# Performance work log

Measured on AMD Instinct MI355X. Metric: run time of the kernel, lower is better.

Reference implementation:

```python
import jax, jax.numpy as jnp
import numpy as np


def _bce_logits(x, t):
    # numerically stable BCEWithLogits (pos_weight=1), elementwise
    return jnp.maximum(x, 0.0) - x * t + jnp.log1p(jnp.exp(-jnp.abs(x)))


def _ciou(box1, box2, eps=1e-9):
    # box1, box2: [n,4] in (cx, cy, w, h); matches bbox_iou(..., x1y1x2y2=False, CIoU=True)
    b1x1, b1x2 = box1[:, 0] - box1[:, 2] / 2, box1[:, 0] + box1[:, 2] / 2
    b1y1, b1y2 = box1[:, 1] - box1[:, 3] / 2, box1[:, 1] + box1[:, 3] / 2
    b2x1, b2x2 = box2[:, 0] - box2[:, 2] / 2, box2[:, 0] + box2[:, 2] / 2
    b2y1, b2y2 = box2[:, 1] - box2[:, 3] / 2, box2[:, 1] + box2[:, 3] / 2
    inter = (jnp.clip(jnp.minimum(b1x2, b2x2) - jnp.maximum(b1x1, b2x1), 0.0)
             * jnp.clip(jnp.minimum(b1y2, b2y2) - jnp.maximum(b1y1, b2y1), 0.0))
    w1, h1 = b1x2 - b1x1, b1y2 - b1y1 + eps
    w2, h2 = b2x2 - b2x1, b2y2 - b2y1 + eps
    union = w1 * h1 + w2 * h2 - inter + eps
    iou = inter / union
    cw = jnp.maximum(b1x2, b2x2) - jnp.minimum(b1x1, b2x1)
    ch = jnp.maximum(b1y2, b2y2) - jnp.minimum(b1y1, b2y1)
    c2 = cw ** 2 + ch ** 2 + eps
    rho2 = ((b2x1 + b2x2 - b1x1 - b1x2) ** 2 + (b2y1 + b2y2 - b1y1 - b1y2) ** 2) / 4.0
    v = (4.0 / jnp.pi ** 2) * (jnp.arctan(w2 / h2) - jnp.arctan(w1 / h1)) ** 2
    alpha = jax.lax.stop_gradient(v / (1.0 + eps - iou + v))  # torch.no_grad()
    return iou - (rho2 / c2 + v * alpha)


def _layer_loss(preds, targets, anchors, li):
    # preds: [B, na, H, W, 5+nc]; targets: [nt,6]; anchors: [n_layers, na, 2]
    B, na, H, W, C = preds.shape
    nt = targets.shape[0]
    ai = jnp.arange(na, dtype=preds.dtype)
    # targets.repeat(na,1,1) with anchor index appended -> [na, nt, 7]
    t7 = jnp.concatenate([jnp.broadcast_to(targets[None], (na, nt, 6)),
                          jnp.broadcast_to(ai[:, None, None], (na, nt, 1))], axis=2)
    gain = jnp.array([1.0, 1.0, W, H, W, H, 1.0], dtype=preds.dtype)
    t = t7 * gain
    # anchor-ratio filter: max(r, 1/r).max(-1) < 4 (as boolean mask instead of fancy-index)
    r = t[:, :, 4:6] / anchors[li][:, None, :]                  # [na, nt, 2]
    mask = jnp.max(jnp.maximum(r, 1.0 / r), axis=2) < 4.0       # [na, nt]
    tf = t.reshape(na * nt, 7)
    m = mask.reshape(-1)
    mf = m.astype(preds.dtype)
    b = tf[:, 0].astype(jnp.int32)
    c = tf[:, 1].astype(jnp.int32)
    gxy = tf[:, 2:4]
    gwh = tf[:, 4:6]
    gij = gxy.astype(jnp.int32)  # .long() truncation (coords >= 0)
    gi = jnp.clip(gij[:, 0], 0, W - 1)
    gj = jnp.clip(gij[:, 1], 0, H - 1)
    a = tf[:, 6].astype(jnp.int32)
    # faithful to original: anch = anchors[a] then forward takes [range(n), a] => anchors[a, a]
    anch = anchors[a, a]
    # img_ids = unique(batch ids).flip(); with full 0..B-1 coverage lookup == B-1-b
    match = (B - 1) - b
    ps = preds[match, a, gj, gi]                                # [na*nt, C] gather
    pxy = jax.nn.sigmoid(ps[:, :2])
    pwh = jnp.exp(ps[:, 2:4]) * anch
    pbox = jnp.concatenate([pxy, pwh], axis=1)
    tbox = jnp.concatenate([gxy - gij.astype(gxy.dtype), gwh], axis=1)
    iou = _ciou(pbox, tbox)
    nvalid = jnp.maximum(mf.sum(), 1.0)
    lbox = ((1.0 - iou) * mf).sum() / nvalid                    # mean over matched targets
    # scatter detached clamped iou into tobj; invalid rows get OOB batch idx -> dropped
    scatter_b = jnp.where(m, match, B)
    tobj = jnp.zeros((B, na, H, W), preds.dtype).at[scatter_b, a, gj, gi].set(
        jax.lax.stop_gradient(jnp.clip(iou, 0.0)) * mf)
    nc = C - 5
    t1h = jax.nn.one_hot(c, nc, dtype=preds.dtype)
    lcls = (_bce_logits(ps[:, 5:], t1h) * mf[:, None]).sum() / (nvalid * nc)
    lobj = _bce_logits(preds[..., 4], tobj).mean()
    return lbox, lobj, lcls


def setup_inputs() -> dict:
    key = jax.random.key(0)
    ks = jax.random.split(key, 6)
    p0 = jax.random.normal(ks[0], (16, 3, 80, 80, 85), jnp.float32)
    p1 = jax.random.normal(ks[1], (16, 3, 40, 40, 85), jnp.float32)
    p2 = jax.random.normal(ks[2], (16, 3, 20, 20, 85), jnp.float32)
    nt, B = 300, 16
    img = (jnp.arange(nt) % B).astype(jnp.float32)  # every batch id present
    cls = jax.random.randint(ks[3], (nt,), 0, 80).astype(jnp.float32)
    xy = jax.random.uniform(ks[4], (nt, 2), minval=0.05, maxval=0.95)
    wh = jax.random.uniform(ks[5], (nt, 2), minval=0.02, maxval=0.2)
    targets = jnp.concatenate([img[:, None], cls[:, None], xy, wh], axis=1)
    anchors = jnp.array([[[1.25, 1.625], [2.0, 3.75], [4.125, 2.875]],
                         [[1.875, 3.8125], [3.875, 2.8125], [3.6875, 7.4375]],
                         [[3.625, 2.8125], [4.875, 6.1875], [11.65625, 10.1875]]],
                        dtype=jnp.float32)
    return {"p0": p0, "p1": p1, "p2": p2, "targets": targets, "anchors": anchors}


def reference(p0, p1, p2, targets, anchors):
    lb = lo = lc = 0.0
    for li, p in enumerate((p0, p1, p2)):
        a_, b_, c_ = _layer_loss(p, targets, anchors, li)
        lb = lb + a_
        lo = lo + b_
        lc = lc + c_
    lbox = lb * 0.05
    lobj = lo * 1.0
    lcls = lc * 0.5
    loss = lbox + lobj + lcls
    stats = jnp.stack([lbox, lobj, lcls, loss])
    return (jnp.reshape(loss, (1,)), stats)
```

## Files before the change

kernel.cpp:

```cpp
#include <hip/hip_runtime.h>
#include <math.h>

#define NT    300
#define NA    3
#define BATCH 16
#define NCLS  80
#define CCH   85
#define NROWS 2700
#define NBO   394
#define NBT   675
#define NBLK  (NBO + NBT)
#define HASHSZ 4096


__device__ __forceinline__ float softplusf(float x) {
    return fmaxf(x, 0.f) + log1pf(expf(-fabsf(x)));
}

__device__ __forceinline__ double block_reduce(double v, double* red) {
    #pragma unroll
    for (int off = 32; off > 0; off >>= 1) v += __shfl_down(v, off, 64);
    const int wid = threadIdx.x >> 6, lane = threadIdx.x & 63;
    if (lane == 0) red[wid] = v;
    __syncthreads();
    double r = (threadIdx.x < 4) ? red[threadIdx.x] : 0.0;
    r += __shfl_down(r, 2, 64);
    r += __shfl_down(r, 1, 64);
    __syncthreads();
    return r;
}

__global__ __launch_bounds__(256) void main_kernel(
    const float* __restrict__ p0, const float* __restrict__ p1,
    const float* __restrict__ p2,
    const float* __restrict__ targets, const float* __restrict__ anchors,
    char* __restrict__ ws)
{
    __shared__ double red[4];

    double* obj_part = (double*)(ws);
    float*  row_lbox = (float*)(ws + 3200);
    float*  row_lcls = (float*)(ws + 14000);
    float*  row_nval = (float*)(ws + 24800);
    int*    row_key  = (int*)(ws + 35600);
    float*  row_val  = (float*)(ws + 46400);

    if (blockIdx.x < NBO) {
        const int ob = blockIdx.x;
        int li, bb;
        if (ob < 300)      { li = 0; bb = ob; }
        else if (ob < 375) { li = 1; bb = ob - 300; }
        else               { li = 2; bb = ob - 375; }
        const float* p = (li == 0) ? p0 : ((li == 1) ? p1 : p2);
        const int N = (BATCH * NA * 6400) >> (2*li);

        float s = 0.f;
        #pragma unroll
        for (int k = 0; k < 4; ++k) {
            const int idx = bb * 1024 + k * 256 + threadIdx.x;
            if (idx < N) s += softplusf(p[(size_t)idx * CCH + 4]);
        }
        const double t = block_reduce((double)s, red);
        if (threadIdx.x == 0) obj_part[ob] = t;
        return;
    }

    const int gr   = (blockIdx.x - NBO) * 4 + (threadIdx.x >> 6);
    const int lane = threadIdx.x & 63;
    const int li   = gr / (NA * NT);
    const int r    = gr - li * (NA * NT);
    const int a    = r / NT;
    const int ti   = r - a * NT;
    const float* p = (li == 0) ? p0 : ((li == 1) ? p1 : p2);
    const int W = 80 >> li, H = W;

    const float img = targets[ti*6 + 0];
    const float cls = targets[ti*6 + 1];
    const float tx  = targets[ti*6 + 2] * (float)W;
    const float ty  = targets[ti*6 + 3] * (float)H;
    const float tw  = targets[ti*6 + 4] * (float)W;
    const float th  = targets[ti*6 + 5] * (float)H;

    const float ax = anchors[(li*3 + a)*2 + 0];
    const float ay = anchors[(li*3 + a)*2 + 1];
    const float rx = tw / ax, ry = th / ay;
    const float mr = fmaxf(fmaxf(rx, 1.f/rx), fmaxf(ry, 1.f/ry));
    const bool  mask = mr < 4.f;
    const float mf = mask ? 1.f : 0.f;

    const int b = (int)img;
    const int c = (int)cls;
    const int gij_x = (int)tx;
    const int gij_y = (int)ty;
    const int gi = min(max(gij_x, 0), W - 1);
    const int gj = min(max(gij_y, 0), H - 1);

    const float anch_x = anchors[(a*3 + a)*2 + 0];
    const float anch_y = anchors[(a*3 + a)*2 + 1];

    const int match = BATCH - 1 - b;
    const int cell  = ((match*NA + a)*H + gj)*W + gi;
    const float* ps = p + (size_t)cell * CCH;

    const float x1 = ps[lane];
    const float x2 = (lane < CCH - 64) ? ps[64 + lane] : 0.f;

    const float s0   = __shfl(x1, 0);
    const float s1   = __shfl(x1, 1);
    const float s2   = __shfl(x1, 2);
    const float s3   = __shfl(x1, 3);
    const float objx = __shfl(x1, 4);

    const int ch = 5 + c;
    float contrib = (lane >= 5) ? softplusf(x1) : 0.f;
    if (lane < CCH - 64) contrib += softplusf(x2);
    if (lane == ch) contrib -= x1;
    if (ch >= 64 && lane == ch - 64) contrib -= x2;
    #pragma unroll
    for (int off = 32; off > 0; off >>= 1)
        contrib += __shfl_down(contrib, off, 64);

    const float pxx = 1.f / (1.f + expf(-s0));
    const float pyy = 1.f / (1.f + expf(-s1));
    const float pw  = expf(s2) * anch_x;
    const float ph  = expf(s3) * anch_y;
    const float fx  = tx - (float)gij_x;
    const float fy  = ty - (float)gij_y;

    const float eps = 1e-9f;
    const float b1x1 = pxx - pw*0.5f, b1x2 = pxx + pw*0.5f;
    const float b1y1 = pyy - ph*0.5f, b1y2 = pyy + ph*0.5f;
    const float b2x1 = fx - tw*0.5f,  b2x2 = fx + tw*0.5f;
    const float b2y1 = fy - th*0.5f,  b2y2 = fy + th*0.5f;
    float iw = fminf(b1x2, b2x2) - fmaxf(b1x1, b2x1); iw = fmaxf(iw, 0.f);
    float ih = fminf(b1y2, b2y2) - fmaxf(b1y1, b2y1); ih = fmaxf(ih, 0.f);
    const float inter = iw * ih;
    const float w1 = b1x2 - b1x1, h1 = b1y2 - b1y1 + eps;
    const float w2 = b2x2 - b2x1, h2 = b2y2 - b2y1 + eps;
    const float uni = w1*h1 + w2*h2 - inter + eps;
    const float iou = inter / uni;
    const float cw  = fmaxf(b1x2, b2x2) - fminf(b1x1, b2x1);
    const float chh = fmaxf(b1y2, b2y2) - fminf(b1y1, b2y1);
    const float c2 = cw*cw + chh*chh + eps;
    const float dx = b2x1 + b2x2 - b1x1 - b1x2;
    const float dy = b2y1 + b2y2 - b1y1 - b1y2;
    const float rho2 = (dx*dx + dy*dy) * 0.25f;
    const float dat = atanf(w2/h2) - atanf(w1/h1);
    const float v = 0.40528473456935108577f * dat * dat;
    const float alpha = v / (1.f + eps - iou + v);
    const float ciou = iou - (rho2/c2 + v*alpha);

    if (lane == 0) {
        row_lbox[gr] = (1.f - ciou) * mf;
        row_lcls[gr] = contrib * mf;
        row_nval[gr] = mf;
        row_key[gr]  = mask ? ((li << 20) | cell) : -1;
        row_val[gr]  = mask ? objx * fmaxf(ciou, 0.f) : 0.f;
    }
}

__global__ __launch_bounds__(256) void final_kernel(
    const char* __restrict__ ws, float* __restrict__ out)
{
    __shared__ double red[4];
    __shared__ int hkey[HASHSZ];
    __shared__ int hrow[HASHSZ];

    const double* obj_part = (const double*)(ws);
    const float*  row_lbox = (const float*)(ws + 3200);
    const float*  row_lcls = (const float*)(ws + 14000);
    const float*  row_nval = (const float*)(ws + 24800);
    const int*    row_key  = (const int*)(ws + 35600);
    const float*  row_val  = (const float*)(ws + 46400);

    for (int q = threadIdx.x; q < HASHSZ; q += 256) { hkey[q] = -1; hrow[q] = -1; }
    __syncthreads();

    double so[3] = {0, 0, 0};
    for (int bk = threadIdx.x; bk < NBO; bk += 256) {
        const double v = obj_part[bk];
        if (bk < 300)      so[0] += v;
        else if (bk < 375) so[1] += v;
        else               so[2] += v;
    }

    int    slots[11];
    int    nm = 0;
    double lb[3] = {0,0,0}, lc[3] = {0,0,0}, nv[3] = {0,0,0}, co[3] = {0,0,0};

    for (int i = threadIdx.x; i < NROWS; i += 256) {
        const int l = i / (NA * NT);
        lb[l] += (double)row_lbox[i];
        lc[l] += (double)row_lcls[i];
        nv[l] += (double)row_nval[i];
        const int k = row_key[i];
        int s = -1;
        if (k >= 0) {
            unsigned h = ((unsigned)k * 2654435761u) >> 20;
            s = (int)(h & (HASHSZ - 1));
            while (true) {
                const int prev = atomicCAS(&hkey[s], -1, k);
                if (prev == -1 || prev == k) { atomicMax(&hrow[s], i); break; }
                s = (s + 1) & (HASHSZ - 1);
            }
        }
        slots[nm++] = s;
    }
    __syncthreads();
    nm = 0;
    for (int i = threadIdx.x; i < NROWS; i += 256) {
        const int s = slots[nm++];
        if (s >= 0 && hrow[s] == i)
            co[i / (NA * NT)] += (double)row_val[i];
    }

    double rsum[12];
    #pragma unroll
    for (int l = 0; l < 3; ++l) {
        rsum[l*4 + 0] = block_reduce(lb[l], red);
        rsum[l*4 + 1] = block_reduce(lc[l], red);
        rsum[l*4 + 2] = block_reduce(co[l], red);
        rsum[l*4 + 3] = block_reduce(nv[l], red);
        so[l]         = block_reduce(so[l], red);
    }

    if (threadIdx.x == 0) {
        double lbox = 0.0, lobj = 0.0, lcls = 0.0;
        for (int l = 0; l < 3; ++l) {
            const double nvv = fmax(rsum[l*4 + 3], 1.0);
            lbox += rsum[l*4 + 0] / nvv;
            lcls += rsum[l*4 + 1] / (nvv * (double)NCLS);
            const double N = (double)((BATCH * NA * 6400) >> (2*l));
            lobj += (so[l] - rsum[l*4 + 2]) / N;
        }
        lbox *= 0.05;
        lcls *= 0.5;
        const double loss = lbox + lobj + lcls;
        out[0] = (float)loss;
        out[1] = (float)lbox;
        out[2] = (float)lobj;
        out[3] = (float)lcls;
        out[4] = (float)loss;
    }
}

extern "C" void kernel_launch(void* const* d_in, const int* in_sizes, int n_in,
                              void* d_out, int out_size, void* d_ws, size_t ws_size,
                              hipStream_t stream) {
    const float* p0      = (const float*)d_in[0];
    const float* p1      = (const float*)d_in[1];
    const float* p2      = (const float*)d_in[2];
    const float* targets = (const float*)d_in[3];
    const float* anchors = (const float*)d_in[4];

    main_kernel<<<NBLK, 256, 0, stream>>>(p0, p1, p2, targets, anchors,
                                          (char*)d_ws);
    final_kernel<<<1, 256, 0, stream>>>((const char*)d_ws, (float*)d_out);
}
```

Before: 182.1 us.

## Merge row work into objectness blocks, pack row data, widen final kernel

Removes the separate row blocks: each of the 394 objectness blocks now also runs up to two target rows per wave after its objectness reduction. Per-row outputs are packed into one float4 plus a key, which cuts the number of global stores and loads. The final single-block kernel grows from 256 to 1024 threads so each thread handles fewer rows and hash insertions. The cost is a longer critical path per block in the main kernel, and 1024-thread reductions with more synchronisation in the final kernel.

```diff
diff --git a/kernel.cpp b/kernel.cpp
--- a/kernel.cpp
+++ b/kernel.cpp
@@ -7,9 +7,8 @@
 #define NCLS  80
 #define CCH   85
 #define NROWS 2700
-#define NBO   394
-#define NBT   675
-#define NBLK  (NBO + NBT)
+#define NBLK  394
+#define NWAVE (NBLK * 4)
 #define HASHSZ 4096
 
 
@@ -17,7 +16,7 @@
     return fmaxf(x, 0.f) + log1pf(expf(-fabsf(x)));
 }
 
-__device__ __forceinline__ double block_reduce(double v, double* red) {
+__device__ __forceinline__ double block_reduce256(double v, double* red) {
     #pragma unroll
     for (int off = 32; off > 0; off >>= 1) v += __shfl_down(v, off, 64);
     const int wid = threadIdx.x >> 6, lane = threadIdx.x & 63;
@@ -26,6 +25,19 @@
     double r = (threadIdx.x < 4) ? red[threadIdx.x] : 0.0;
     r += __shfl_down(r, 2, 64);
     r += __shfl_down(r, 1, 64);
+    __syncthreads();
+    return r;
+}
+
+__device__ __forceinline__ double block_reduce1024(double v, double* red) {
+    #pragma unroll
+    for (int off = 32; off > 0; off >>= 1) v += __shfl_down(v, off, 64);
+    const int wid = threadIdx.x >> 6, lane = threadIdx.x & 63;
+    if (lane == 0) red[wid] = v;
+    __syncthreads();
+    double r = (threadIdx.x < 16) ? red[threadIdx.x] : 0.0;
+    #pragma unroll
+    for (int off = 8; off > 0; off >>= 1) r += __shfl_down(r, off, 64);
     __syncthreads();
     return r;
 }
@@ -39,13 +51,10 @@
     __shared__ double red[4];
 
     double* obj_part = (double*)(ws);
-    float*  row_lbox = (float*)(ws + 3200);
-    float*  row_lcls = (float*)(ws + 14000);
-    float*  row_nval = (float*)(ws + 24800);
-    int*    row_key  = (int*)(ws + 35600);
-    float*  row_val  = (float*)(ws + 46400);
-
-    if (blockIdx.x < NBO) {
+    float4* row_data = (float4*)(ws + 3200);
+    int*    row_key  = (int*)(ws + 46400);
+
+    {
         const int ob = blockIdx.x;
         int li, bb;
         if (ob < 300)      { li = 0; bb = ob; }
@@ -60,139 +69,144 @@
             const int idx = bb * 1024 + k * 256 + threadIdx.x;
             if (idx < N) s += softplusf(p[(size_t)idx * CCH + 4]);
         }
-        const double t = block_reduce((double)s, red);
+        const double t = block_reduce256((double)s, red);
         if (threadIdx.x == 0) obj_part[ob] = t;
-        return;
-    }
-
-    const int gr   = (blockIdx.x - NBO) * 4 + (threadIdx.x >> 6);
+    }
+
+    const int gw   = blockIdx.x * 4 + (threadIdx.x >> 6);
     const int lane = threadIdx.x & 63;
-    const int li   = gr / (NA * NT);
-    const int r    = gr - li * (NA * NT);
-    const int a    = r / NT;
-    const int ti   = r - a * NT;
-    const float* p = (li == 0) ? p0 : ((li == 1) ? p1 : p2);
-    const int W = 80 >> li, H = W;
-
-    const float img = targets[ti*6 + 0];
-    const float cls = targets[ti*6 + 1];
-    const float tx  = targets[ti*6 + 2] * (float)W;
-    const float ty  = targets[ti*6 + 3] * (float)H;
-    const float tw  = targets[ti*6 + 4] * (float)W;
-    const float th  = targets[ti*6 + 5] * (float)H;
-
-    const float ax = anchors[(li*3 + a)*2 + 0];
-    const float ay = anchors[(li*3 + a)*2 + 1];
-    const float rx = tw / ax, ry = th / ay;
-    const float mr = fmaxf(fmaxf(rx, 1.f/rx), fmaxf(ry, 1.f/ry));
-    const bool  mask = mr < 4.f;
-    const float mf = mask ? 1.f : 0.f;
-
-    const int b = (int)img;
-    const int c = (int)cls;
-    const int gij_x = (int)tx;
-    const int gij_y = (int)ty;
-    const int gi = min(max(gij_x, 0), W - 1);
-    const int gj = min(max(gij_y, 0), H - 1);
-
-    const float anch_x = anchors[(a*3 + a)*2 + 0];
-    const float anch_y = anchors[(a*3 + a)*2 + 1];
-
-    const int match = BATCH - 1 - b;
-    const int cell  = ((match*NA + a)*H + gj)*W + gi;
-    const float* ps = p + (size_t)cell * CCH;
-
-    const float x1 = ps[lane];
-    const float x2 = (lane < CCH - 64) ? ps[64 + lane] : 0.f;
-
-    const float s0   = __shfl(x1, 0);
-    const float s1   = __shfl(x1, 1);
-    const float s2   = __shfl(x1, 2);
-    const float s3   = __shfl(x1, 3);
-    const float objx = __shfl(x1, 4);
-
-    const int ch = 5 + c;
-    float contrib = (lane >= 5) ? softplusf(x1) : 0.f;
-    if (lane < CCH - 64) contrib += softplusf(x2);
-    if (lane == ch) contrib -= x1;
-    if (ch >= 64 && lane == ch - 64) contrib -= x2;
-    #pragma unroll
-    for (int off = 32; off > 0; off >>= 1)
-        contrib += __shfl_down(contrib, off, 64);
-
-    const float pxx = 1.f / (1.f + expf(-s0));
-    const float pyy = 1.f / (1.f + expf(-s1));
-    const float pw  = expf(s2) * anch_x;
-    const float ph  = expf(s3) * anch_y;
-    const float fx  = tx - (float)gij_x;
-    const float fy  = ty - (float)gij_y;
-
-    const float eps = 1e-9f;
-    const float b1x1 = pxx - pw*0.5f, b1x2 = pxx + pw*0.5f;
-    const float b1y1 = pyy - ph*0.5f, b1y2 = pyy + ph*0.5f;
-    const float b2x1 = fx - tw*0.5f,  b2x2 = fx + tw*0.5f;
-    const float b2y1 = fy - th*0.5f,  b2y2 = fy + th*0.5f;
-    float iw = fminf(b1x2, b2x2) - fmaxf(b1x1, b2x1); iw = fmaxf(iw, 0.f);
-    float ih = fminf(b1y2, b2y2) - fmaxf(b1y1, b2y1); ih = fmaxf(ih, 0.f);
-    const float inter = iw * ih;
-    const float w1 = b1x2 - b1x1, h1 = b1y2 - b1y1 + eps;
-    const float w2 = b2x2 - b2x1, h2 = b2y2 - b2y1 + eps;
-    const float uni = w1*h1 + w2*h2 - inter + eps;
-    const float iou = inter / uni;
-    const float cw  = fmaxf(b1x2, b2x2) - fminf(b1x1, b2x1);
-    const float chh = fmaxf(b1y2, b2y2) - fminf(b1y1, b2y1);
-    const float c2 = cw*cw + chh*chh + eps;
-    const float dx = b2x1 + b2x2 - b1x1 - b1x2;
-    const float dy = b2y1 + b2y2 - b1y1 - b1y2;
-    const float rho2 = (dx*dx + dy*dy) * 0.25f;
-    const float dat = atanf(w2/h2) - atanf(w1/h1);
-    const float v = 0.40528473456935108577f * dat * dat;
-    const float alpha = v / (1.f + eps - iou + v);
-    const float ciou = iou - (rho2/c2 + v*alpha);
-
-    if (lane == 0) {
-        row_lbox[gr] = (1.f - ciou) * mf;
-        row_lcls[gr] = contrib * mf;
-        row_nval[gr] = mf;
-        row_key[gr]  = mask ? ((li << 20) | cell) : -1;
-        row_val[gr]  = mask ? objx * fmaxf(ciou, 0.f) : 0.f;
-    }
-}
-
-__global__ __launch_bounds__(256) void final_kernel(
+
+    #pragma unroll
+    for (int rr = 0; rr < 2; ++rr) {
+        const int gr = gw + rr * NWAVE;
+        if (gr >= NROWS) break;
+        const int li = gr / (NA * NT);
+        const int r  = gr - li * (NA * NT);
+        const int a  = r / NT;
+        const int ti = r - a * NT;
+        const float* p = (li == 0) ? p0 : ((li == 1) ? p1 : p2);
+        const int W = 80 >> li, H = W;
+
+        const float img = targets[ti*6 + 0];
+        const float cls = targets[ti*6 + 1];
+        const float tx  = targets[ti*6 + 2] * (float)W;
+        const float ty  = targets[ti*6 + 3] * (float)H;
+        const float tw  = targets[ti*6 + 4] * (float)W;
+        const float th  = targets[ti*6 + 5] * (float)H;
+
+        const float ax = anchors[(li*3 + a)*2 + 0];
+        const float ay = anchors[(li*3 + a)*2 + 1];
+        const float rx = tw / ax, ry = th / ay;
+        const float mr = fmaxf(fmaxf(rx, 1.f/rx), fmaxf(ry, 1.f/ry));
+        const bool  mask = mr < 4.f;
+        const float mf = mask ? 1.f : 0.f;
+
+        const int b = (int)img;
+        const int c = (int)cls;
+        const int gij_x = (int)tx;
+        const int gij_y = (int)ty;
+        const int gi = min(max(gij_x, 0), W - 1);
+        const int gj = min(max(gij_y, 0), H - 1);
+
+        const float anch_x = anchors[(a*3 + a)*2 + 0];
+        const float anch_y = anchors[(a*3 + a)*2 + 1];
+
+        const int match = BATCH - 1 - b;
+        const int cell  = ((match*NA + a)*H + gj)*W + gi;
+        const float* ps = p + (size_t)cell * CCH;
+
+        const float x1 = ps[lane];
+        const float x2 = (lane < CCH - 64) ? ps[64 + lane] : 0.f;
+
+        const float s0   = __shfl(x1, 0);
+        const float s1   = __shfl(x1, 1);
+        const float s2   = __shfl(x1, 2);
+        const float s3   = __shfl(x1, 3);
+        const float objx = __shfl(x1, 4);
+
+        const int ch = 5 + c;
+        float contrib = (lane >= 5) ? softplusf(x1) : 0.f;
+        if (lane < CCH - 64) contrib += softplusf(x2);
+        if (lane == ch) contrib -= x1;
+        if (ch >= 64 && lane == ch - 64) contrib -= x2;
+        #pragma unroll
+        for (int off = 32; off > 0; off >>= 1)
+            contrib += __shfl_down(contrib, off, 64);
+
+        const float pxx = 1.f / (1.f + expf(-s0));
+        const float pyy = 1.f / (1.f + expf(-s1));
+        const float pw  = expf(s2) * anch_x;
+        const float ph  = expf(s3) * anch_y;
+        const float fx  = tx - (float)gij_x;
+        const float fy  = ty - (float)gij_y;
+
+        const float eps = 1e-9f;
+        const float b1x1 = pxx - pw*0.5f, b1x2 = pxx + pw*0.5f;
+        const float b1y1 = pyy - ph*0.5f, b1y2 = pyy + ph*0.5f;
+        const float b2x1 = fx - tw*0.5f,  b2x2 = fx + tw*0.5f;
+        const float b2y1 = fy - th*0.5f,  b2y2 = fy + th*0.5f;
+        float iw = fminf(b1x2, b2x2) - fmaxf(b1x1, b2x1); iw = fmaxf(iw, 0.f);
+        float ih = fminf(b1y2, b2y2) - fmaxf(b1y1, b2y1); ih = fmaxf(ih, 0.f);
+        const float inter = iw * ih;
+        const float w1 = b1x2 - b1x1, h1 = b1y2 - b1y1 + eps;
+        const float w2 = b2x2 - b2x1, h2 = b2y2 - b2y1 + eps;
+        const float uni = w1*h1 + w2*h2 - inter + eps;
+        const float iou = inter / uni;
+        const float cw  = fmaxf(b1x2, b2x2) - fminf(b1x1, b2x1);
+        const float chh = fmaxf(b1y2, b2y2) - fminf(b1y1, b2y1);
+        const float c2 = cw*cw + chh*chh + eps;
+        const float dx = b2x1 + b2x2 - b1x1 - b1x2;
+        const float dy = b2y1 + b2y2 - b1y1 - b1y2;
+        const float rho2 = (dx*dx + dy*dy) * 0.25f;
+        const float dat = atanf(w2/h2) - atanf(w1/h1);
+        const float v = 0.40528473456935108577f * dat * dat;
+        const float alpha = v / (1.f + eps - iou + v);
+        const float ciou = iou - (rho2/c2 + v*alpha);
+
+        if (lane == 0) {
+            row_data[gr] = make_float4((1.f - ciou) * mf,
+                                       contrib * mf,
+                                       mf,
+                                       mask ? objx * fmaxf(ciou, 0.f) : 0.f);
+            row_key[gr]  = mask ? ((li << 20) | cell) : -1;
+        }
+    }
+}
+
+__global__ __launch_bounds__(1024) void final_kernel(
     const char* __restrict__ ws, float* __restrict__ out)
 {
-    __shared__ double red[4];
+    __shared__ double red[16];
     __shared__ int hkey[HASHSZ];
     __shared__ int hrow[HASHSZ];
 
     const double* obj_part = (const double*)(ws);
-    const float*  row_lbox = (const float*)(ws + 3200);
-    const float*  row_lcls = (const float*)(ws + 14000);
-    const float*  row_nval = (const float*)(ws + 24800);
-    const int*    row_key  = (const int*)(ws + 35600);
-    const float*  row_val  = (const float*)(ws + 46400);
-
-    for (int q = threadIdx.x; q < HASHSZ; q += 256) { hkey[q] = -1; hrow[q] = -1; }
+    const float4* row_data = (const float4*)(ws + 3200);
+    const int*    row_key  = (const int*)(ws + 46400);
+
+    for (int q = threadIdx.x; q < HASHSZ; q += 1024) { hkey[q] = -1; hrow[q] = -1; }
     __syncthreads();
 
     double so[3] = {0, 0, 0};
-    for (int bk = threadIdx.x; bk < NBO; bk += 256) {
-        const double v = obj_part[bk];
-        if (bk < 300)      so[0] += v;
-        else if (bk < 375) so[1] += v;
-        else               so[2] += v;
-    }
-
-    int    slots[11];
+    if (threadIdx.x < NBLK) {
+        const double v = obj_part[threadIdx.x];
+        if (threadIdx.x < 300)      so[0] = v;
+        else if (threadIdx.x < 375) so[1] = v;
+        else                        so[2] = v;
+    }
+
+    int    slots[3];
+    float4 rdat[3];
     int    nm = 0;
     double lb[3] = {0,0,0}, lc[3] = {0,0,0}, nv[3] = {0,0,0}, co[3] = {0,0,0};
 
-    for (int i = threadIdx.x; i < NROWS; i += 256) {
+    for (int i = threadIdx.x; i < NROWS; i += 1024) {
         const int l = i / (NA * NT);
-        lb[l] += (double)row_lbox[i];
-        lc[l] += (double)row_lcls[i];
-        nv[l] += (double)row_nval[i];
+        const float4 d = row_data[i];
+        rdat[nm] = d;
+        lb[l] += (double)d.x;
+        lc[l] += (double)d.y;
+        nv[l] += (double)d.z;
         const int k = row_key[i];
         int s = -1;
         if (k >= 0) {
@@ -208,20 +222,21 @@
     }
     __syncthreads();
     nm = 0;
-    for (int i = threadIdx.x; i < NROWS; i += 256) {
-        const int s = slots[nm++];
+    for (int i = threadIdx.x; i < NROWS; i += 1024) {
+        const int s = slots[nm];
         if (s >= 0 && hrow[s] == i)
-            co[i / (NA * NT)] += (double)row_val[i];
+            co[i / (NA * NT)] += (double)rdat[nm].w;
+        ++nm;
     }
 
     double rsum[12];
     #pragma unroll
     for (int l = 0; l < 3; ++l) {
-        rsum[l*4 + 0] = block_reduce(lb[l], red);
-        rsum[l*4 + 1] = block_reduce(lc[l], red);
-        rsum[l*4 + 2] = block_reduce(co[l], red);
-        rsum[l*4 + 3] = block_reduce(nv[l], red);
-        so[l]         = block_reduce(so[l], red);
+        rsum[l*4 + 0] = block_reduce1024(lb[l], red);
+        rsum[l*4 + 1] = block_reduce1024(lc[l], red);
+        rsum[l*4 + 2] = block_reduce1024(co[l], red);
+        rsum[l*4 + 3] = block_reduce1024(nv[l], red);
+        so[l]         = block_reduce1024(so[l], red);
     }
 
     if (threadIdx.x == 0) {
@@ -255,5 +270,5 @@
 
     main_kernel<<<NBLK, 256, 0, stream>>>(p0, p1, p2, targets, anchors,
                                           (char*)d_ws);
-    final_kernel<<<1, 256, 0, stream>>>((const char*)d_ws, (float*)d_out);
-}
+    final_kernel<<<1, 1024, 0, stream>>>((const char*)d_ws, (float*)d_out);
+}
```

Result: slower. 190.6 us (+4.7%).
